# Kernel tuning notes

Hardware: AMD Instinct MI355X
Metric: run time of the kernel (lower is better)

The kernel has to match this reference:

```python
import jax, jax.numpy as jnp
import numpy as np

B, S, E, H, DK, DV = 2, 2048, 1024, 16, 64, 64
NEG = -1e9


def setup_inputs() -> dict:
    key = jax.random.key(0)
    ks = jax.random.split(key, 12)
    s = 0.02
    return {
        "query": jax.random.normal(ks[0], (B, S, E), jnp.float32),
        "key": jax.random.normal(ks[1], (B, S, E), jnp.float32),
        "value": jax.random.normal(ks[2], (B, S, E), jnp.float32),
        "mask": jax.random.randint(ks[3], (B, S, S), 0, 2, jnp.int32),
        "Wq": jax.random.normal(ks[4], (E, H * DK), jnp.float32) * s,
        "bq": jnp.zeros((H * DK,), jnp.float32),
        "Wk": jax.random.normal(ks[5], (E, H * DK), jnp.float32) * s,
        "bk": jnp.zeros((H * DK,), jnp.float32),
        "Wv": jax.random.normal(ks[6], (E, H * DV), jnp.float32) * s,
        "bv": jnp.zeros((H * DV,), jnp.float32),
        "Wo": jax.random.normal(ks[7], (H * DV, E), jnp.float32) * s,
        "bo": jnp.zeros((E,), jnp.float32),
    }


def reference(query, key, value, mask, Wq, bq, Wk, bk, Wv, bv, Wo, bo):
    # projections, then split heads: (B,S,H*D) -> (B,H,S,D)
    q = (query @ Wq + bq).reshape(B, S, H, DK).transpose(0, 2, 1, 3)
    k = (key @ Wk + bk).reshape(B, S, H, DK).transpose(0, 2, 1, 3)
    v = (value @ Wv + bv).reshape(B, S, H, DV).transpose(0, 2, 1, 3)
    scores = jnp.einsum("bhqd,bhkd->bhqk", q, k) / jnp.sqrt(jnp.float32(DK))
    scores = jnp.where(mask[:, None, :, :] == 0, jnp.float32(NEG), scores)
    weights = jax.nn.softmax(scores, axis=-1)
    ctx = jnp.einsum("bhqk,bhkd->bhqd", weights, v)
    ctx = ctx.transpose(0, 2, 1, 3).reshape(B, S, H * DV)
    return ctx @ Wo + bo
```

## Files before the change

### kernel.cpp

```cpp
#include <hip/hip_runtime.h>

typedef __attribute__((ext_vector_type(8))) short s16x8;
typedef __attribute__((ext_vector_type(4))) float f32x4;
typedef __attribute__((ext_vector_type(16))) float f32x16;
typedef unsigned short u16;
typedef unsigned int u32;
typedef unsigned long long u64;

__device__ __forceinline__ u16 f2bf(float f) {
  u32 u = __builtin_bit_cast(u32, f);
  u += 0x7fff + ((u >> 16) & 1);
  return (u16)(u >> 16);
}

__device__ __forceinline__ float exp2fast(float x) {
#if __has_builtin(__builtin_amdgcn_exp2f)
  return __builtin_amdgcn_exp2f(x);
#else
  return __expf(x * 0.6931471805599453f);
#endif
}

__device__ __forceinline__ void gload16(const void* g, void* l) {
  __builtin_amdgcn_global_load_lds((const __attribute__((address_space(1))) u32*)g,
                                   (__attribute__((address_space(3))) u32*)l, 16, 0, 0);
}

#define MFMA(a, b, c) __builtin_amdgcn_mfma_f32_16x16x32_bf16((a), (b), (c), 0, 0, 0)
#define MFMA32(a, b, c) __builtin_amdgcn_mfma_f32_32x32x16_bf16((a), (b), (c), 0, 0, 0)

#define QSCALE 0.18033688011112042f

__global__ __launch_bounds__(256) void cvt_bf16_3(const float* __restrict__ q,
                                                  const float* __restrict__ k,
                                                  const float* __restrict__ v,
                                                  u16* __restrict__ oq, u16* __restrict__ ok,
                                                  u16* __restrict__ ov) {
  int z = blockIdx.y;
  const float* src = (z == 0) ? q : (z == 1) ? k : v;
  u16* dst = (z == 0) ? oq : (z == 1) ? ok : ov;
  int i = blockIdx.x * 256 + threadIdx.x;
  const float4* s4 = (const float4*)src;
  float4 a = s4[2 * i], b = s4[2 * i + 1];
  uint4 o;
  o.x = (u32)f2bf(a.x) | ((u32)f2bf(a.y) << 16);
  o.y = (u32)f2bf(a.z) | ((u32)f2bf(a.w) << 16);
  o.z = (u32)f2bf(b.x) | ((u32)f2bf(b.y) << 16);
  o.w = (u32)f2bf(b.z) | ((u32)f2bf(b.w) << 16);
  ((uint4*)dst)[i] = o;
}

__global__ __launch_bounds__(256) void mask_bits(const int* __restrict__ mask,
                                                 u64* __restrict__ mb) {
  int wi = (blockIdx.x * 256 + threadIdx.x) >> 6;
  int lane = threadIdx.x & 63;
  u64 bits = __ballot(mask[((size_t)wi << 6) + lane] != 0);
  if (lane == 0) mb[wi] = bits;
}

__global__ __launch_bounds__(256) void transpose_w4(const float* __restrict__ W0,
                                                    const float* __restrict__ W1,
                                                    const float* __restrict__ W2,
                                                    const float* __restrict__ W3,
                                                    u16* __restrict__ T0, u16* __restrict__ T1,
                                                    u16* __restrict__ T2, u16* __restrict__ T3) {
  int z = blockIdx.z;
  const float* W = (z == 0) ? W0 : (z == 1) ? W1 : (z == 2) ? W2 : W3;
  u16* WT = (z == 0) ? T0 : (z == 1) ? T1 : (z == 2) ? T2 : T3;
  __shared__ float t[32][33];
  int tx = threadIdx.x, ty = threadIdx.y;
  int n = blockIdx.x * 32 + tx;
#pragma unroll
  for (int j = 0; j < 4; j++) {
    int k = blockIdx.y * 32 + ty + 8 * j;
    t[ty + 8 * j][tx] = W[(size_t)k * 1024 + n];
  }
  __syncthreads();
  int k = blockIdx.y * 32 + tx;
#pragma unroll
  for (int j = 0; j < 4; j++) {
    int n2 = blockIdx.x * 32 + ty + 8 * j;
    WT[(size_t)n2 * 1024 + k] = f2bf(t[tx][ty + 8 * j]);
  }
}

template <int BM, int BN>
__device__ __forceinline__ void gemm_core(const u16* __restrict__ A, const u16* __restrict__ BT,
                                          int m0, int n0, u16* Ash, u16* Bsh,
                                          f32x4 (&acc)[BM / 32][BN / 32]) {
  constexpr int MF = BM / 32, NF = BN / 32;
  constexpr int BATCH = BM / 32 + BN / 32;
  const int tid = threadIdx.x;
  const int lane = tid & 63, wid = tid >> 6;
  const int r16 = lane & 15, g = lane >> 4;
  const int wm = wid >> 1, wn = wid & 1;
  const int swz = r16 & 7;
  const f32x4 vz = {0.f, 0.f, 0.f, 0.f};
#pragma unroll
  for (int mf = 0; mf < MF; mf++)
#pragma unroll
    for (int nf = 0; nf < NF; nf++) acc[mf][nf] = vz;

  auto stage = [&](int buf, int k0) {
#pragma unroll
    for (int i = 0; i < MF; i++) {
      int ch = i * 256 + tid;
      int row = ch >> 3, sc = (ch & 7) ^ (row & 7);
      gload16(A + (((size_t)(m0 + row)) << 10) + k0 + sc * 8,
              Ash + (size_t)buf * (BM * 64) + ch * 8);
    }
#pragma unroll
    for (int i = 0; i < NF; i++) {
      int ch = i * 256 + tid;
      int row = ch >> 3, sc = (ch & 7) ^ (row & 7);
      gload16(BT + (((size_t)(n0 + row)) << 10) + k0 + sc * 8,
              Bsh + (size_t)buf * (BN * 64) + ch * 8);
    }
  };

  asm volatile("" ::: "memory");
  stage(0, 0);
  asm volatile("" ::: "memory");
  stage(1, 64);
  asm volatile("" ::: "memory");

  for (int t = 0; t < 16; t++) {
    const int cur = t & 1;
    if (t == 15) {
      asm volatile("s_waitcnt vmcnt(0)" ::: "memory");
    } else if constexpr (BATCH == 8) {
      asm volatile("s_waitcnt vmcnt(8)" ::: "memory");
    } else {
      asm volatile("s_waitcnt vmcnt(6)" ::: "memory");
    }
    asm volatile("s_barrier" ::: "memory");

    const u16* Acur = Ash + (size_t)cur * (BM * 64);
    const u16* Bcur = Bsh + (size_t)cur * (BN * 64);
    __builtin_amdgcn_s_setprio(1);
#pragma unroll
    for (int kk = 0; kk < 2; kk++) {
      const int c = (kk * 4 + g);
      s16x8 af[MF], bfr[NF];
#pragma unroll
      for (int mf = 0; mf < MF; mf++)
        af[mf] = *(const s16x8*)(Acur + ((wm * (BM / 2) + mf * 16 + r16) << 6) +
                                 ((c ^ swz) << 3));
#pragma unroll
      for (int nf = 0; nf < NF; nf++)
        bfr[nf] = *(const s16x8*)(Bcur + ((wn * (BN / 2) + nf * 16 + r16) << 6) +
                                  ((c ^ swz) << 3));
#pragma unroll
      for (int mf = 0; mf < MF; mf++)
#pragma unroll
        for (int nf = 0; nf < NF; nf++) acc[mf][nf] = MFMA(af[mf], bfr[nf], acc[mf][nf]);
    }
    __builtin_amdgcn_s_setprio(0);

    asm volatile("s_barrier" ::: "memory");
    if (t + 2 < 16) stage(cur, (t + 2) * 64);
  }
}

__global__ __launch_bounds__(256, 2) void proj_gemm(
    const u16* __restrict__ Xq, const u16* __restrict__ Xk, const u16* __restrict__ Xv,
    const u16* __restrict__ WqT, const u16* __restrict__ WkT, const u16* __restrict__ WvT,
    const float* __restrict__ bq, const float* __restrict__ bk, const float* __restrict__ bv,
    u16* __restrict__ Qo, u16* __restrict__ Ko, u16* __restrict__ Vto) {
  __shared__ u16 Ash[2 * 128 * 64], Bsh[2 * 128 * 64];
  const int z = blockIdx.z;
  const u16* A = (z == 0) ? Xq : (z == 1) ? Xk : Xv;
  const u16* BT = (z == 0) ? WqT : (z == 1) ? WkT : WvT;
  const float* bias = (z == 0) ? bq : (z == 1) ? bk : bv;
  u16* O = (z == 0) ? Qo : (z == 1) ? Ko : Vto;
  const float sc = (z == 0) ? QSCALE : 1.0f;
  const int m0 = blockIdx.y * 128, n0 = blockIdx.x * 128;
  f32x4 acc[4][4];
  gemm_core<128, 128>(A, BT, m0, n0, Ash, Bsh, acc);
  const int tid = threadIdx.x, lane = tid & 63, wid = tid >> 6;
  const int r16 = lane & 15, g = lane >> 4, wm = wid >> 1, wn = wid & 1;
#pragma unroll
  for (int nf = 0; nf < 4; nf++) {
    int col = n0 + wn * 64 + nf * 16 + r16;
    float bb = bias[col];
    int h = col >> 6, d = col & 63;
#pragma unroll
    for (int mf = 0; mf < 4; mf++) {
#pragma unroll
      for (int ri = 0; ri < 4; ri++) {
        int row = m0 + wm * 64 + mf * 16 + g * 4 + ri;
        int b_ = row >> 11, s_ = row & 2047;
        u16 val = f2bf((acc[mf][nf][ri] + bb) * sc);
        if (z < 2)
          O[((((size_t)b_ * 16 + h) * 2048 + s_) << 6) + d] = val;
        else
          O[((((size_t)b_ * 16 + h) * 64 + d) << 11) + s_] = val;
      }
    }
  }
}

__global__ __launch_bounds__(256, 2) void out_gemm(const u16* __restrict__ ctx,
                                                   const u16* __restrict__ WoT,
                                                   const float* __restrict__ bo,
                                                   float* __restrict__ out) {
  __shared__ u16 Ash[2 * 64 * 64], Bsh[2 * 128 * 64];
  const int m0 = blockIdx.y * 64, n0 = blockIdx.x * 128;
  f32x4 acc[2][4];
  gemm_core<64, 128>(ctx, WoT, m0, n0, Ash, Bsh, acc);
  const int tid = threadIdx.x, lane = tid & 63, wid = tid >> 6;
  const int r16 = lane & 15, g = lane >> 4, wm = wid >> 1, wn = wid & 1;
#pragma unroll
  for (int nf = 0; nf < 4; nf++) {
    int col = n0 + wn * 64 + nf * 16 + r16;
    float bb = bo[col];
#pragma unroll
    for (int mf = 0; mf < 2; mf++) {
#pragma unroll
      for (int ri = 0; ri < 4; ri++) {
        int row = m0 + wm * 32 + mf * 16 + g * 4 + ri;
        out[((size_t)row << 10) + col] = acc[mf][nf][ri] + bb;
      }
    }
  }
}

__device__ __forceinline__ s16x8 pack4u(u32 a0, u32 a1, u32 b0, u32 b1) {
  union { u32 u[4]; s16x8 v; } p;
  p.u[0] = a0; p.u[1] = a1; p.u[2] = b0; p.u[3] = b1;
  return p.v;
}

__device__ __forceinline__ void softpack(const f32x16& sv, u32 wm, s16x8& pA, s16x8& pB) {
  float e[16];
#pragma unroll
  for (int qd = 0; qd < 4; qd++)
#pragma unroll
    for (int j = 0; j < 4; j++)
      e[qd * 4 + j] = exp2fast(sv[qd * 4 + j]) * (float)((wm >> (qd * 8 + j)) & 1);
#pragma unroll
  for (int n = 0; n < 2; n++) {
    u32 a0, a1, b0, b1;
    asm("v_cvt_pk_bf16_f32 %0, %1, %2" : "=v"(a0) : "v"(e[n * 8 + 0]), "v"(e[n * 8 + 1]));
    asm("v_cvt_pk_bf16_f32 %0, %1, %2" : "=v"(a1) : "v"(e[n * 8 + 2]), "v"(e[n * 8 + 3]));
    asm("v_cvt_pk_bf16_f32 %0, %1, %2" : "=v"(b0) : "v"(e[n * 8 + 4]), "v"(e[n * 8 + 5]));
    asm("v_cvt_pk_bf16_f32 %0, %1, %2" : "=v"(b1) : "v"(e[n * 8 + 6]), "v"(e[n * 8 + 7]));
    asm("v_permlane32_swap_b32 %0, %1" : "+v"(a0), "+v"(b0));
    asm("v_permlane32_swap_b32 %0, %1" : "+v"(a1), "+v"(b1));
    if (n == 0) pA = pack4u(a0, a1, b0, b1);
    else        pB = pack4u(a0, a1, b0, b1);
  }
}

__global__ __launch_bounds__(256, 2) void flash_attn(const u16* __restrict__ Q,
                                                     const u16* __restrict__ K,
                                                     const u16* __restrict__ Vt,
                                                     const u64* __restrict__ Mb64,
                                                     u16* __restrict__ ctx) {
  __shared__ __align__(16) u16 Ksh[2][64][64];
  __shared__ __align__(16) u16 Vsh[2][64][64];

  const int tid = threadIdx.x, w = tid >> 6, lane = tid & 63;
  const int l31 = lane & 31, h5 = lane >> 5, l7 = lane & 7;

  int work = ((int)blockIdx.x & 7) * 64 + ((int)blockIdx.x >> 3);
  const int qt = work & 15, bh = work >> 4;
  const int b = bh >> 4, h = bh & 15;
  const int q0 = qt * 128 + w * 32;

  const u16* Qb = Q + ((size_t)bh << 17);
  const u16* Kb = K + ((size_t)bh << 17);
  const u16* Vb = Vt + ((size_t)bh << 17);
  const u64* Mrow = Mb64 + ((size_t)(b * 2048 + q0 + l31) << 5);

  const int srow = tid >> 3, sk16 = tid & 7;
#define STAGE(buf, kv0)                                                                   \
  {                                                                                       \
    _Pragma("unroll") for (int i = 0; i < 2; i++) {                                       \
      int row = i * 32 + srow;                                                            \
      int sc = sk16 ^ (row & 7);                                                          \
      gload16(Kb + (((size_t)((kv0) + row)) << 6) + sc * 8,                               \
              (char*)&Ksh[buf][0][0] + (i * 256 + tid) * 16);                             \
      gload16(Vb + (((size_t)row) << 11) + (kv0) + sc * 8,                                \
              (char*)&Vsh[buf][0][0] + (i * 256 + tid) * 16);                             \
    }                                                                                     \
  }

  s16x8 aq[4];
#pragma unroll
  for (int dk = 0; dk < 4; dk++)
    aq[dk] = *(const s16x8*)(Qb + ((q0 + l31) << 6) + dk * 16 + h5 * 8);
  asm volatile("" ::: "memory");
  STAGE(0, 0);
  u64 mcur = Mrow[0];
  asm volatile("" ::: "memory");
  STAGE(1, 64);
  u64 mnext = Mrow[1];
  asm volatile("" ::: "memory");

  s16x8 vones;
#pragma unroll
  for (int j = 0; j < 8; j++) vones[j] = (short)0x3F80;

  f32x16 o0, o1, o4;
#pragma unroll
  for (int r = 0; r < 16; r++) { o0[r] = 0.f; o1[r] = 0.f; o4[r] = 0.f; }

  for (int t = 0; t < 32; t++) {
    const int cur = t & 1;
    if (t == 31) {
      asm volatile("s_waitcnt vmcnt(0)" ::: "memory");
    } else {
      asm volatile("s_waitcnt vmcnt(5)" ::: "memory");
    }
    asm volatile("s_barrier" ::: "memory");

    const u16* Kc = &Ksh[cur][0][0];
    const u16* Vc = &Vsh[cur][0][0];

    f32x16 s0, s1;
#pragma unroll
    for (int r = 0; r < 16; r++) { s0[r] = 0.f; s1[r] = 0.f; }
    __builtin_amdgcn_s_setprio(1);
#pragma unroll
    for (int dk = 0; dk < 4; dk++) {
      int ch = (((dk << 1) + h5) ^ l7) << 3;
      s16x8 ak0 = *(const s16x8*)(Kc + (l31 << 6) + ch);
      s16x8 ak1 = *(const s16x8*)(Kc + ((32 + l31) << 6) + ch);
      s0 = MFMA32(ak0, aq[dk], s0);
      s1 = MFMA32(ak1, aq[dk], s1);
    }
    __builtin_amdgcn_s_setprio(0);

    u64 msh = mcur >> (h5 << 2);
    s16x8 pa[4];
    softpack(s0, (u32)msh, pa[0], pa[1]);
    softpack(s1, (u32)(msh >> 32), pa[2], pa[3]);

    __builtin_amdgcn_s_setprio(1);
#pragma unroll
    for (int km = 0; km < 4; km++) {
      int ch = (((km << 1) + h5) ^ l7) << 3;
      s16x8 bv0 = *(const s16x8*)(Vc + (l31 << 6) + ch);
      s16x8 bv1 = *(const s16x8*)(Vc + ((32 + l31) << 6) + ch);
      o0 = MFMA32(pa[km], bv0, o0);
      o1 = MFMA32(pa[km], bv1, o1);
      o4 = MFMA32(pa[km], vones, o4);
    }
    __builtin_amdgcn_s_setprio(0);

    asm volatile("s_barrier" ::: "memory");
    u64 mnew = 0;
    if (t + 2 < 32) {
      STAGE(cur, (t + 2) * 64);
      mnew = Mrow[t + 2];
    }
    mcur = mnext;
    mnext = mnew;
  }
#undef STAGE

#pragma unroll
  for (int r = 0; r < 16; r++) {
    int qr = (r & 3) + 8 * (r >> 2) + 4 * h5;
    size_t rowoff = ((size_t)((b << 11) + q0 + qr)) << 10;
    float iv = 1.f / o4[r];
    ctx[rowoff + (h << 6) + l31]      = f2bf(o0[r] * iv);
    ctx[rowoff + (h << 6) + 32 + l31] = f2bf(o1[r] * iv);
  }
}

extern "C" void kernel_launch(void* const* d_in, const int* in_sizes, int n_in,
                              void* d_out, int out_size, void* d_ws, size_t ws_size,
                              hipStream_t stream) {
  const float* query = (const float*)d_in[0];
  const float* key_  = (const float*)d_in[1];
  const float* value = (const float*)d_in[2];
  const int*   mask  = (const int*)d_in[3];
  const float* Wq = (const float*)d_in[4];
  const float* bq = (const float*)d_in[5];
  const float* Wk = (const float*)d_in[6];
  const float* bk = (const float*)d_in[7];
  const float* Wv = (const float*)d_in[8];
  const float* bv = (const float*)d_in[9];
  const float* Wo = (const float*)d_in[10];
  const float* bo = (const float*)d_in[11];

  const size_t MB = 1048576;
  char* ws = (char*)d_ws;
  u16* Xq  = (u16*)(ws + 0 * MB);
  u16* Xk  = (u16*)(ws + 8 * MB);
  u16* Xv  = (u16*)(ws + 16 * MB);
  u16* WqT = (u16*)(ws + 24 * MB);
  u16* WkT = (u16*)(ws + 26 * MB);
  u16* WvT = (u16*)(ws + 28 * MB);
  u16* WoT = (u16*)(ws + 30 * MB);
  u16* Qd  = (u16*)(ws + 32 * MB);
  u16* Kd  = (u16*)(ws + 40 * MB);
  u16* Vtd = (u16*)(ws + 48 * MB);
  u16* ctx = (u16*)(ws + 56 * MB);
  u64* Mb  = (u64*)(ws + 72 * MB);

  cvt_bf16_3<<<dim3(2048, 3), 256, 0, stream>>>(query, key_, value, Xq, Xk, Xv);
  mask_bits<<<32768, 256, 0, stream>>>(mask, Mb);

  dim3 tb(32, 8);
  transpose_w4<<<dim3(32, 32, 4), tb, 0, stream>>>(Wq, Wk, Wv, Wo, WqT, WkT, WvT, WoT);

  proj_gemm<<<dim3(8, 32, 3), 256, 0, stream>>>(Xq, Xk, Xv, WqT, WkT, WvT, bq, bk, bv,
                                                Qd, Kd, Vtd);
  flash_attn<<<512, 256, 0, stream>>>(Qd, Kd, Vtd, Mb, ctx);
  out_gemm<<<dim3(8, 64), 256, 0, stream>>>(ctx, WoT, bo, (float*)d_out);
}
```

Measured before the change: 157.4 us.

## Software-pipeline attention loop: defer softmax and PV MFMA by one tile

```diff
diff --git a/kernel.cpp b/kernel.cpp
--- a/kernel.cpp
+++ b/kernel.cpp
@@ -292,19 +292,23 @@
     aq[dk] = *(const s16x8*)(Qb + ((q0 + l31) << 6) + dk * 16 + h5 * 8);
   asm volatile("" ::: "memory");
   STAGE(0, 0);
-  u64 mcur = Mrow[0];
+  u64 m_c = Mrow[0];
   asm volatile("" ::: "memory");
   STAGE(1, 64);
-  u64 mnext = Mrow[1];
-  asm volatile("" ::: "memory");
-
-  s16x8 vones;
-#pragma unroll
-  for (int j = 0; j < 8; j++) vones[j] = (short)0x3F80;
-
-  f32x16 o0, o1, o4;
-#pragma unroll
-  for (int r = 0; r < 16; r++) { o0[r] = 0.f; o1[r] = 0.f; o4[r] = 0.f; }
+  u64 m_n = Mrow[1];
+  asm volatile("" ::: "memory");
+  u64 m_pp = 0;
+
+  s16x8 vones, z8;
+#pragma unroll
+  for (int j = 0; j < 8; j++) { vones[j] = (short)0x3F80; z8[j] = 0; }
+
+  f32x16 o0, o1, o4, sp0, sp1;
+#pragma unroll
+  for (int r = 0; r < 16; r++) { o0[r] = 0.f; o1[r] = 0.f; o4[r] = 0.f; sp0[r] = 0.f; sp1[r] = 0.f; }
+  s16x8 vrA[4], vrB[4];
+#pragma unroll
+  for (int km = 0; km < 4; km++) { vrA[km] = z8; vrB[km] = z8; }
 
   for (int t = 0; t < 32; t++) {
     const int cur = t & 1;
@@ -332,33 +336,50 @@
     }
     __builtin_amdgcn_s_setprio(0);
 
-    u64 msh = mcur >> (h5 << 2);
+    u64 msh = m_pp >> (h5 << 2);
     s16x8 pa[4];
-    softpack(s0, (u32)msh, pa[0], pa[1]);
-    softpack(s1, (u32)(msh >> 32), pa[2], pa[3]);
+    softpack(sp0, (u32)msh, pa[0], pa[1]);
+    softpack(sp1, (u32)(msh >> 32), pa[2], pa[3]);
 
     __builtin_amdgcn_s_setprio(1);
+#pragma unroll
+    for (int km = 0; km < 4; km++) {
+      o0 = MFMA32(pa[km], vrA[km], o0);
+      o1 = MFMA32(pa[km], vrB[km], o1);
+      o4 = MFMA32(pa[km], vones, o4);
+    }
+    __builtin_amdgcn_s_setprio(0);
+
 #pragma unroll
     for (int km = 0; km < 4; km++) {
       int ch = (((km << 1) + h5) ^ l7) << 3;
-      s16x8 bv0 = *(const s16x8*)(Vc + (l31 << 6) + ch);
-      s16x8 bv1 = *(const s16x8*)(Vc + ((32 + l31) << 6) + ch);
-      o0 = MFMA32(pa[km], bv0, o0);
-      o1 = MFMA32(pa[km], bv1, o1);
-      o4 = MFMA32(pa[km], vones, o4);
-    }
-    __builtin_amdgcn_s_setprio(0);
-
+      vrA[km] = *(const s16x8*)(Vc + (l31 << 6) + ch);
+      vrB[km] = *(const s16x8*)(Vc + ((32 + l31) << 6) + ch);
+    }
+    asm volatile("s_waitcnt lgkmcnt(0)" ::: "memory");
     asm volatile("s_barrier" ::: "memory");
-    u64 mnew = 0;
+    u64 m_new = 0;
     if (t + 2 < 32) {
       STAGE(cur, (t + 2) * 64);
-      mnew = Mrow[t + 2];
-    }
-    mcur = mnext;
-    mnext = mnew;
+      m_new = Mrow[t + 2];
+    }
+    m_pp = m_c; m_c = m_n; m_n = m_new;
+    sp0 = s0; sp1 = s1;
   }
 #undef STAGE
+
+  {
+    u64 msh = m_pp >> (h5 << 2);
+    s16x8 pa[4];
+    softpack(sp0, (u32)msh, pa[0], pa[1]);
+    softpack(sp1, (u32)(msh >> 32), pa[2], pa[3]);
+#pragma unroll
+    for (int km = 0; km < 4; km++) {
+      o0 = MFMA32(pa[km], vrA[km], o0);
+      o1 = MFMA32(pa[km], vrB[km], o1);
+      o4 = MFMA32(pa[km], vones, o4);
+    }
+  }
 
 #pragma unroll
   for (int r = 0; r < 16; r++) {
```

New measurement: 156.9 us. Within noise of the previous version (-0.3%).

## Process two KV tiles per iteration and compute row sums with VALU

Applied to the files above, without the earlier changes.

```diff
diff --git a/kernel.cpp b/kernel.cpp
--- a/kernel.cpp
+++ b/kernel.cpp
@@ -231,7 +231,11 @@
   return p.v;
 }
 
-__device__ __forceinline__ void softpack(const f32x16& sv, u32 wm, s16x8& pA, s16x8& pB) {
+__device__ __forceinline__ float bflo(u32 pk) { return __builtin_bit_cast(float, pk << 16); }
+__device__ __forceinline__ float bfhi(u32 pk) { return __builtin_bit_cast(float, pk & 0xFFFF0000u); }
+
+__device__ __forceinline__ void softpack(const f32x16& sv, u32 wm, s16x8& pA, s16x8& pB,
+                                         float& rs) {
   float e[16];
 #pragma unroll
   for (int qd = 0; qd < 4; qd++)
@@ -245,6 +249,8 @@
     asm("v_cvt_pk_bf16_f32 %0, %1, %2" : "=v"(a1) : "v"(e[n * 8 + 2]), "v"(e[n * 8 + 3]));
     asm("v_cvt_pk_bf16_f32 %0, %1, %2" : "=v"(b0) : "v"(e[n * 8 + 4]), "v"(e[n * 8 + 5]));
     asm("v_cvt_pk_bf16_f32 %0, %1, %2" : "=v"(b1) : "v"(e[n * 8 + 6]), "v"(e[n * 8 + 7]));
+    rs += ((bflo(a0) + bfhi(a0)) + (bflo(a1) + bfhi(a1))) +
+          ((bflo(b0) + bfhi(b0)) + (bflo(b1) + bfhi(b1)));
     asm("v_permlane32_swap_b32 %0, %1" : "+v"(a0), "+v"(b0));
     asm("v_permlane32_swap_b32 %0, %1" : "+v"(a1), "+v"(b1));
     if (n == 0) pA = pack4u(a0, a1, b0, b1);
@@ -257,8 +263,8 @@
                                                      const u16* __restrict__ Vt,
                                                      const u64* __restrict__ Mb64,
                                                      u16* __restrict__ ctx) {
-  __shared__ __align__(16) u16 Ksh[2][64][64];
-  __shared__ __align__(16) u16 Vsh[2][64][64];
+  __shared__ __align__(16) u16 Ksh[4][64][64];
+  __shared__ __align__(16) u16 Vsh[4][64][64];
 
   const int tid = threadIdx.x, w = tid >> 6, lane = tid & 63;
   const int l31 = lane & 31, h5 = lane >> 5, l7 = lane & 7;
@@ -292,79 +298,102 @@
     aq[dk] = *(const s16x8*)(Qb + ((q0 + l31) << 6) + dk * 16 + h5 * 8);
   asm volatile("" ::: "memory");
   STAGE(0, 0);
-  u64 mcur = Mrow[0];
-  asm volatile("" ::: "memory");
   STAGE(1, 64);
-  u64 mnext = Mrow[1];
-  asm volatile("" ::: "memory");
-
-  s16x8 vones;
-#pragma unroll
-  for (int j = 0; j < 8; j++) vones[j] = (short)0x3F80;
-
-  f32x16 o0, o1, o4;
-#pragma unroll
-  for (int r = 0; r < 16; r++) { o0[r] = 0.f; o1[r] = 0.f; o4[r] = 0.f; }
-
-  for (int t = 0; t < 32; t++) {
-    const int cur = t & 1;
-    if (t == 31) {
+  u64 m_c0 = Mrow[0], m_c1 = Mrow[1];
+  asm volatile("" ::: "memory");
+  STAGE(2, 128);
+  STAGE(3, 192);
+  u64 m_n0 = Mrow[2], m_n1 = Mrow[3];
+  asm volatile("" ::: "memory");
+
+  f32x16 o0, o1;
+#pragma unroll
+  for (int r = 0; r < 16; r++) { o0[r] = 0.f; o1[r] = 0.f; }
+  float rs = 0.f;
+
+  for (int t = 0; t < 16; t++) {
+    const int base = (t & 1) * 2;
+    if (t == 15) {
       asm volatile("s_waitcnt vmcnt(0)" ::: "memory");
     } else {
-      asm volatile("s_waitcnt vmcnt(5)" ::: "memory");
+      asm volatile("s_waitcnt vmcnt(10)" ::: "memory");
     }
     asm volatile("s_barrier" ::: "memory");
 
-    const u16* Kc = &Ksh[cur][0][0];
-    const u16* Vc = &Vsh[cur][0][0];
-
-    f32x16 s0, s1;
-#pragma unroll
-    for (int r = 0; r < 16; r++) { s0[r] = 0.f; s1[r] = 0.f; }
+    const u16* KcA = &Ksh[base][0][0];
+    const u16* KcB = &Ksh[base + 1][0][0];
+    const u16* VcA = &Vsh[base][0][0];
+    const u16* VcB = &Vsh[base + 1][0][0];
+
+    f32x16 s0, s1, s2, s3;
+#pragma unroll
+    for (int r = 0; r < 16; r++) { s0[r] = 0.f; s1[r] = 0.f; s2[r] = 0.f; s3[r] = 0.f; }
     __builtin_amdgcn_s_setprio(1);
 #pragma unroll
     for (int dk = 0; dk < 4; dk++) {
       int ch = (((dk << 1) + h5) ^ l7) << 3;
-      s16x8 ak0 = *(const s16x8*)(Kc + (l31 << 6) + ch);
-      s16x8 ak1 = *(const s16x8*)(Kc + ((32 + l31) << 6) + ch);
-      s0 = MFMA32(ak0, aq[dk], s0);
-      s1 = MFMA32(ak1, aq[dk], s1);
+      s16x8 akA0 = *(const s16x8*)(KcA + (l31 << 6) + ch);
+      s16x8 akA1 = *(const s16x8*)(KcA + ((32 + l31) << 6) + ch);
+      s16x8 akB0 = *(const s16x8*)(KcB + (l31 << 6) + ch);
+      s16x8 akB1 = *(const s16x8*)(KcB + ((32 + l31) << 6) + ch);
+      s0 = MFMA32(akA0, aq[dk], s0);
+      s1 = MFMA32(akA1, aq[dk], s1);
+      s2 = MFMA32(akB0, aq[dk], s2);
+      s3 = MFMA32(akB1, aq[dk], s3);
     }
     __builtin_amdgcn_s_setprio(0);
 
-    u64 msh = mcur >> (h5 << 2);
+    u64 mshA = m_c0 >> (h5 << 2);
     s16x8 pa[4];
-    softpack(s0, (u32)msh, pa[0], pa[1]);
-    softpack(s1, (u32)(msh >> 32), pa[2], pa[3]);
-
+    softpack(s0, (u32)mshA, pa[0], pa[1], rs);
+    softpack(s1, (u32)(mshA >> 32), pa[2], pa[3], rs);
     __builtin_amdgcn_s_setprio(1);
 #pragma unroll
     for (int km = 0; km < 4; km++) {
       int ch = (((km << 1) + h5) ^ l7) << 3;
-      s16x8 bv0 = *(const s16x8*)(Vc + (l31 << 6) + ch);
-      s16x8 bv1 = *(const s16x8*)(Vc + ((32 + l31) << 6) + ch);
+      s16x8 bv0 = *(const s16x8*)(VcA + (l31 << 6) + ch);
+      s16x8 bv1 = *(const s16x8*)(VcA + ((32 + l31) << 6) + ch);
       o0 = MFMA32(pa[km], bv0, o0);
       o1 = MFMA32(pa[km], bv1, o1);
-      o4 = MFMA32(pa[km], vones, o4);
     }
     __builtin_amdgcn_s_setprio(0);
 
+    u64 mshB = m_c1 >> (h5 << 2);
+    s16x8 pb[4];
+    softpack(s2, (u32)mshB, pb[0], pb[1], rs);
+    softpack(s3, (u32)(mshB >> 32), pb[2], pb[3], rs);
+    __builtin_amdgcn_s_setprio(1);
+#pragma unroll
+    for (int km = 0; km < 4; km++) {
+      int ch = (((km << 1) + h5) ^ l7) << 3;
+      s16x8 bv0 = *(const s16x8*)(VcB + (l31 << 6) + ch);
+      s16x8 bv1 = *(const s16x8*)(VcB + ((32 + l31) << 6) + ch);
+      o0 = MFMA32(pb[km], bv0, o0);
+      o1 = MFMA32(pb[km], bv1, o1);
+    }
+    __builtin_amdgcn_s_setprio(0);
+
     asm volatile("s_barrier" ::: "memory");
-    u64 mnew = 0;
-    if (t + 2 < 32) {
-      STAGE(cur, (t + 2) * 64);
-      mnew = Mrow[t + 2];
-    }
-    mcur = mnext;
-    mnext = mnew;
+    u64 mw0 = 0, mw1 = 0;
+    if (t + 2 < 16) {
+      STAGE(base, (2 * t + 4) * 64);
+      STAGE(base + 1, (2 * t + 5) * 64);
+      mw0 = Mrow[2 * t + 4];
+      mw1 = Mrow[2 * t + 5];
+    }
+    m_c0 = m_n0; m_c1 = m_n1;
+    m_n0 = mw0;  m_n1 = mw1;
   }
 #undef STAGE
+
+  rs += __shfl_xor(rs, 32, 64);
+  float inv = 1.f / rs;
 
 #pragma unroll
   for (int r = 0; r < 16; r++) {
     int qr = (r & 3) + 8 * (r >> 2) + 4 * h5;
+    float iv = __shfl(inv, qr, 64);
     size_t rowoff = ((size_t)((b << 11) + q0 + qr)) << 10;
-    float iv = 1.f / o4[r];
     ctx[rowoff + (h << 6) + l31]      = f2bf(o0[r] * iv);
     ctx[rowoff + (h << 6) + 32 + l31] = f2bf(o1[r] * iv);
   }
```

Result: no change. 157.9 us (+0.3%).
